# Performance work log

Hardware: AMD Instinct MI355X
Metric: run time of the kernel (lower is better)

## Reference

```python
import jax, jax.numpy as jnp
import numpy as np

B, N_OBJ, FEAT_IN = 512, 3, 2048
FEAT_SIZE = 512
EMBED = 512
HID = 512
VOCAB = 4096
MAX_LEN = 40
T = MAX_LEN - 2  # sampled steps between SOS and appended EOS
SOS_IDX, EOS_IDX = 1, 2
TAU = 1.0


def setup_inputs() -> dict:
    key = jax.random.key(0)
    ks = jax.random.split(key, 16)
    s = lambda k, shape, fan: jax.random.normal(k, shape, jnp.float32) / np.sqrt(fan)
    feats = jax.random.normal(ks[0], (B, N_OBJ, FEAT_IN), jnp.float32)
    targets = jax.random.randint(ks[1], (B,), 0, N_OBJ)
    feat_W = s(ks[2], (FEAT_SIZE, FEAT_IN), FEAT_IN)
    feat_b = jnp.zeros((FEAT_SIZE,), jnp.float32)
    emb_W = s(ks[3], (VOCAB, EMBED), EMBED)
    init_W = s(ks[4], (HID, N_OBJ * (FEAT_SIZE + 1)), N_OBJ * (FEAT_SIZE + 1))
    init_b = jnp.zeros((HID,), jnp.float32)
    gru_Wih = s(ks[5], (3 * HID, EMBED), EMBED)
    gru_Whh = s(ks[6], (3 * HID, HID), HID)
    gru_bih = jnp.zeros((3 * HID,), jnp.float32)
    gru_bhh = jnp.zeros((3 * HID,), jnp.float32)
    out_W = s(ks[7], (VOCAB, HID), HID)
    out_b = jnp.zeros((VOCAB,), jnp.float32)
    # pre-sampled gumbel noise for the T decode steps
    u = jax.random.uniform(ks[8], (T, B, VOCAB), jnp.float32, 1e-10, 1.0)
    gumbel = -jnp.log(-jnp.log(u))
    return dict(feats=feats, targets=targets, feat_W=feat_W, feat_b=feat_b,
                emb_W=emb_W, init_W=init_W, init_b=init_b,
                gru_Wih=gru_Wih, gru_Whh=gru_Whh, gru_bih=gru_bih,
                gru_bhh=gru_bhh, out_W=out_W, out_b=out_b, gumbel=gumbel)


def _gru_cell(x, h, Wih, Whh, bih, bhh):
    gi = x @ Wih.T + bih              # [B, 3H]
    gh = h @ Whh.T + bhh
    i_r, i_z, i_n = jnp.split(gi, 3, axis=-1)
    h_r, h_z, h_n = jnp.split(gh, 3, axis=-1)
    r = jax.nn.sigmoid(i_r + h_r)
    z = jax.nn.sigmoid(i_z + h_z)
    n = jnp.tanh(i_n + r * h_n)
    return (1.0 - z) * n + z * h


def _decode(feats, targets, feat_W, feat_b, emb_W, init_W, init_b,
            gru_Wih, gru_Whh, gru_bih, gru_bhh, out_W, out_b, gumbel):
    bsz = feats.shape[0]
    # embed_features: linear feat model per object + target one-hot
    fe = jnp.einsum('boi,hi->boh', feats, feat_W) + feat_b      # [B,3,F]
    t_oh = jax.nn.one_hot(targets, N_OBJ, dtype=feats.dtype)    # [B,3]
    ft = jnp.concatenate([fe, t_oh[:, :, None]], axis=2).reshape(bsz, -1)
    h0 = ft @ init_W.T + init_b                                  # [B,H]

    sos_oh = jax.nn.one_hot(jnp.full((bsz,), SOS_IDX), VOCAB, dtype=feats.dtype)
    x0 = sos_oh @ emb_W                                          # [B,E]
    done0 = jnp.zeros((bsz,), bool)
    len0 = jnp.ones((bsz,), jnp.int32)                           # counts SOS

    def step(carry, g):
        h, x, done, length = carry
        h = _gru_cell(x, h, gru_Wih, gru_Whh, gru_bih, gru_bhh)
        logits = h @ out_W.T + out_b                             # [B,V]
        soft = jax.nn.softmax((logits + g) / TAU, axis=-1)
        pred = jnp.argmax(soft, axis=-1)
        hard = jax.nn.one_hot(pred, VOCAB, dtype=soft.dtype)
        oh = hard + soft - jax.lax.stop_gradient(soft)           # straight-through
        length = length + (~done).astype(jnp.int32)
        done = done | (pred == EOS_IDX)
        x = oh @ emb_W
        return (h, x, done, length), oh

    (_, _, done, length), ohs = jax.lax.scan(step, (h0, x0, done0, len0), gumbel)
    length = length + (~done).astype(jnp.int32)                  # appended EOS

    eos_oh = jax.nn.one_hot(jnp.full((bsz,), EOS_IDX), VOCAB, dtype=feats.dtype)
    lang = jnp.concatenate(
        [sos_oh[:, None], jnp.transpose(ohs, (1, 0, 2)), eos_oh[:, None]], axis=1)
    mask = (jnp.arange(MAX_LEN)[None, :] < length[:, None])      # zero past length
    lang = lang * mask[:, :, None].astype(lang.dtype)
    return lang, length


def reference(feats, targets, feat_W, feat_b, emb_W, init_W, init_b,
              gru_Wih, gru_Whh, gru_bih, gru_bhh, out_W, out_b, gumbel):
    lang, length = _decode(feats, targets, feat_W, feat_b, emb_W, init_W, init_b,
                           gru_Wih, gru_Whh, gru_bih, gru_bhh, out_W, out_b, gumbel)
    eos_loss = jnp.float32(0.0)
    return lang, length, eos_loss
```

## Files before the change

kernel.cpp:

```cpp
#include <hip/hip_runtime.h>
#include <cstdint>
#include <cstddef>

#define BATCH   512
#define HIDDEN  512
#define EMB     512
#define VOCAB   4096
#define NOBJ    3
#define FEATIN  2048
#define FEATSZ  512
#define MAXLEN  40
#define TSTEPS  38
#define SOS     1
#define EOS     2
#define GIH     1536

#define BK 16
#define BM 64

static __device__ __forceinline__ unsigned long long pack_key(float v, int col) {
    uint32_t u = __float_as_uint(v);
    u = (u & 0x80000000u) ? ~u : (u | 0x80000000u);
    return ((unsigned long long)u << 32) | (uint32_t)(VOCAB - 1 - col);
}

__global__ __launch_bounds__(256) void k_zero(float* __restrict__ out, int n,
                                              unsigned long long* __restrict__ keys) {
    size_t i = (size_t)blockIdx.x * 256 + threadIdx.x;
    size_t i4 = i * 4;
    if (i4 + 3 < (size_t)n) {
        *(float4*)&out[i4] = make_float4(0.f, 0.f, 0.f, 0.f);
    } else if (i4 < (size_t)n) {
        for (size_t j = i4; j < (size_t)n; ++j) out[j] = 0.f;
    }
    if (i < (size_t)TSTEPS * BATCH) keys[i] = 0ULL;
}

__global__ __launch_bounds__(256) void k_fe(const float* __restrict__ feats,
                                            const float* __restrict__ featW,
                                            const float* __restrict__ featb,
                                            float* __restrict__ fe) {
    __shared__ float As[BK][BM];
    __shared__ float Bs[BK][BM];
    const int tid = threadIdx.x;
    const int m0 = blockIdx.y * BM, n0 = blockIdx.x * BM;
    const int tx = tid & 15, ty = tid >> 4;
    const int lrow = tid >> 2, lk = (tid & 3) << 2;
    float acc[4][4] = {};
    for (int k0 = 0; k0 < FEATIN; k0 += BK) {
        float4 a = *(const float4*)&feats[(size_t)(m0 + lrow) * FEATIN + k0 + lk];
        float4 b = *(const float4*)&featW[(size_t)(n0 + lrow) * FEATIN + k0 + lk];
        __syncthreads();
        As[lk+0][lrow] = a.x; As[lk+1][lrow] = a.y; As[lk+2][lrow] = a.z; As[lk+3][lrow] = a.w;
        Bs[lk+0][lrow] = b.x; Bs[lk+1][lrow] = b.y; Bs[lk+2][lrow] = b.z; Bs[lk+3][lrow] = b.w;
        __syncthreads();
#pragma unroll
        for (int kk = 0; kk < BK; ++kk) {
            float4 av = *(const float4*)&As[kk][ty * 4];
            float4 bv = *(const float4*)&Bs[kk][tx * 4];
            float ar[4] = {av.x, av.y, av.z, av.w};
            float br[4] = {bv.x, bv.y, bv.z, bv.w};
#pragma unroll
            for (int i = 0; i < 4; ++i)
#pragma unroll
                for (int j = 0; j < 4; ++j) acc[i][j] += ar[i] * br[j];
        }
    }
#pragma unroll
    for (int i = 0; i < 4; ++i) {
        int r = m0 + ty * 4 + i;
#pragma unroll
        for (int j = 0; j < 4; ++j) {
            int c = n0 + tx * 4 + j;
            fe[(size_t)r * FEATSZ + c] = acc[i][j] + featb[c];
        }
    }
}

__global__ __launch_bounds__(256) void k_h0(const float* __restrict__ fe,
                                            const float* __restrict__ initW,
                                            const float* __restrict__ initb,
                                            const int* __restrict__ targets,
                                            float* __restrict__ h) {
    __shared__ float As[BK][BM];
    __shared__ float Bs[BK][BM];
    const int tid = threadIdx.x;
    const int m0 = blockIdx.y * BM, n0 = blockIdx.x * BM;
    const int tx = tid & 15, ty = tid >> 4;
    const int lrow = tid >> 2, lk = (tid & 3) << 2;
    float acc[4][4] = {};
    const int K = NOBJ * FEATSZ;
    for (int k0 = 0; k0 < K; k0 += BK) {
        float4 a = *(const float4*)&fe[(size_t)(m0 + lrow) * K + k0 + lk];
        float breg[4];
#pragma unroll
        for (int i = 0; i < 4; ++i) {
            int ka = k0 + lk + i;
            breg[i] = initW[(size_t)(n0 + lrow) * 1539 + ka + (ka >> 9)];
        }
        __syncthreads();
        As[lk+0][lrow] = a.x; As[lk+1][lrow] = a.y; As[lk+2][lrow] = a.z; As[lk+3][lrow] = a.w;
#pragma unroll
        for (int i = 0; i < 4; ++i) Bs[lk + i][lrow] = breg[i];
        __syncthreads();
#pragma unroll
        for (int kk = 0; kk < BK; ++kk) {
            float4 av = *(const float4*)&As[kk][ty * 4];
            float4 bv = *(const float4*)&Bs[kk][tx * 4];
            float ar[4] = {av.x, av.y, av.z, av.w};
            float br[4] = {bv.x, bv.y, bv.z, bv.w};
#pragma unroll
            for (int i = 0; i < 4; ++i)
#pragma unroll
                for (int j = 0; j < 4; ++j) acc[i][j] += ar[i] * br[j];
        }
    }
#pragma unroll
    for (int i = 0; i < 4; ++i) {
        int r = m0 + ty * 4 + i;
        int tg = targets[r];
#pragma unroll
        for (int j = 0; j < 4; ++j) {
            int c = n0 + tx * 4 + j;
            h[(size_t)r * HIDDEN + c] =
                acc[i][j] + initb[c] + initW[(size_t)c * 1539 + tg * 513 + 512];
        }
    }
}

__global__ __launch_bounds__(256) void k_P(const float* __restrict__ embW,
                                           const float* __restrict__ Wih,
                                           float* __restrict__ P) {
    __shared__ __align__(16) float As[2][BK][BM + 4];
    __shared__ __align__(16) float Bs[2][BK][128 + 4];
    const int tid = threadIdx.x;
    const int arow = tid >> 2, ak = (tid & 3) << 2;
    const int tx = tid & 15, ty = tid >> 4;
    const int m0 = blockIdx.y * BM, n0 = blockIdx.x * 128;
    const float* Ap = embW + (size_t)(m0 + arow) * EMB;
    const float* Bp0 = Wih + (size_t)(n0 + arow) * EMB;
    const float* Bp1 = Wih + (size_t)(n0 + 64 + arow) * EMB;
    float4 aR = *(const float4*)&Ap[ak];
    float4 bR0 = *(const float4*)&Bp0[ak];
    float4 bR1 = *(const float4*)&Bp1[ak];
    float acc[4][8] = {};
    int buf = 0;
    for (int k0 = 0; k0 < EMB; k0 += BK) {
        As[buf][ak+0][arow] = aR.x; As[buf][ak+1][arow] = aR.y;
        As[buf][ak+2][arow] = aR.z; As[buf][ak+3][arow] = aR.w;
        Bs[buf][ak+0][arow] = bR0.x; Bs[buf][ak+1][arow] = bR0.y;
        Bs[buf][ak+2][arow] = bR0.z; Bs[buf][ak+3][arow] = bR0.w;
        Bs[buf][ak+0][arow+64] = bR1.x; Bs[buf][ak+1][arow+64] = bR1.y;
        Bs[buf][ak+2][arow+64] = bR1.z; Bs[buf][ak+3][arow+64] = bR1.w;
        __syncthreads();
        if (k0 + BK < EMB) {
            aR  = *(const float4*)&Ap[k0 + BK + ak];
            bR0 = *(const float4*)&Bp0[k0 + BK + ak];
            bR1 = *(const float4*)&Bp1[k0 + BK + ak];
        }
#pragma unroll
        for (int kk = 0; kk < BK; ++kk) {
            float4 av  = *(const float4*)&As[buf][kk][ty * 4];
            float4 bv0 = *(const float4*)&Bs[buf][kk][tx * 4];
            float4 bv1 = *(const float4*)&Bs[buf][kk][64 + tx * 4];
            float ar[4] = {av.x, av.y, av.z, av.w};
            float br[8] = {bv0.x, bv0.y, bv0.z, bv0.w, bv1.x, bv1.y, bv1.z, bv1.w};
#pragma unroll
            for (int i = 0; i < 4; ++i)
#pragma unroll
                for (int j = 0; j < 8; ++j) acc[i][j] += ar[i] * br[j];
        }
        buf ^= 1;
    }
#pragma unroll
    for (int i = 0; i < 4; ++i) {
        int r = m0 + ty * 4 + i;
        *(float4*)&P[(size_t)r * GIH + n0 + tx * 4] =
            make_float4(acc[i][0], acc[i][1], acc[i][2], acc[i][3]);
        *(float4*)&P[(size_t)r * GIH + n0 + 64 + tx * 4] =
            make_float4(acc[i][4], acc[i][5], acc[i][6], acc[i][7]);
    }
}

__global__ __launch_bounds__(256) void k_gatesH(const float* __restrict__ h,
                                                const float* __restrict__ Whh,
                                                float* __restrict__ Gh) {
    __shared__ __align__(16) float As[2][BK][BM + 4];
    __shared__ __align__(16) float Bs[2][BK][BM + 4];
    const int tid = threadIdx.x;
    const int arow = tid >> 2, ak = (tid & 3) << 2;
    const int tx = tid & 15, ty = tid >> 4;
    const int m0 = blockIdx.y * BM, n0 = blockIdx.x * BM;
    const float* Ap = h + (size_t)(m0 + arow) * HIDDEN;
    const float* Bp = Whh + (size_t)(n0 + arow) * HIDDEN;
    float4 aR = *(const float4*)&Ap[ak];
    float4 bR = *(const float4*)&Bp[ak];
    float acc[4][4] = {};
    int buf = 0;
    for (int k0 = 0; k0 < HIDDEN; k0 += BK) {
        As[buf][ak+0][arow] = aR.x; As[buf][ak+1][arow] = aR.y;
        As[buf][ak+2][arow] = aR.z; As[buf][ak+3][arow] = aR.w;
        Bs[buf][ak+0][arow] = bR.x; Bs[buf][ak+1][arow] = bR.y;
        Bs[buf][ak+2][arow] = bR.z; Bs[buf][ak+3][arow] = bR.w;
        __syncthreads();
        if (k0 + BK < HIDDEN) {
            aR = *(const float4*)&Ap[k0 + BK + ak];
            bR = *(const float4*)&Bp[k0 + BK + ak];
        }
#pragma unroll
        for (int kk = 0; kk < BK; ++kk) {
            float4 av = *(const float4*)&As[buf][kk][ty * 4];
            float4 bv = *(const float4*)&Bs[buf][kk][tx * 4];
            float ar[4] = {av.x, av.y, av.z, av.w};
            float br[4] = {bv.x, bv.y, bv.z, bv.w};
#pragma unroll
            for (int i = 0; i < 4; ++i)
#pragma unroll
                for (int j = 0; j < 4; ++j) acc[i][j] += ar[i] * br[j];
        }
        buf ^= 1;
    }
#pragma unroll
    for (int i = 0; i < 4; ++i) {
        int r = m0 + ty * 4 + i;
        *(float4*)&Gh[(size_t)r * GIH + n0 + tx * 4] =
            make_float4(acc[i][0], acc[i][1], acc[i][2], acc[i][3]);
    }
}

__global__ __launch_bounds__(256) void k_gru(const float* __restrict__ Gh,
                                             const float* __restrict__ P,
                                             const float* __restrict__ bih,
                                             const float* __restrict__ bhh,
                                             const unsigned long long* __restrict__ keys_prev,
                                             float* __restrict__ h) {
    int idx = blockIdx.x * 256 + threadIdx.x;
    int b = idx >> 7;
    int j4 = (idx & 127) << 2;
    int tok = SOS;
    if (keys_prev) tok = (VOCAB - 1) - (int)(uint32_t)(keys_prev[b] & 0xffffffffULL);
    const float* Pr = P + (size_t)tok * GIH;
    const float* Gr = Gh + (size_t)b * GIH;
    float4 ir = *(const float4*)&Pr[j4];
    float4 iz = *(const float4*)&Pr[j4 + HIDDEN];
    float4 in_ = *(const float4*)&Pr[j4 + 2 * HIDDEN];
    float4 hr = *(const float4*)&Gr[j4];
    float4 hz = *(const float4*)&Gr[j4 + HIDDEN];
    float4 hn = *(const float4*)&Gr[j4 + 2 * HIDDEN];
    float4 bir = *(const float4*)&bih[j4];
    float4 biz = *(const float4*)&bih[j4 + HIDDEN];
    float4 bin = *(const float4*)&bih[j4 + 2 * HIDDEN];
    float4 bhr = *(const float4*)&bhh[j4];
    float4 bhz = *(const float4*)&bhh[j4 + HIDDEN];
    float4 bhn = *(const float4*)&bhh[j4 + 2 * HIDDEN];
    float4 ho = *(const float4*)&h[(size_t)b * HIDDEN + j4];
    float irr[4] = {ir.x + bir.x, ir.y + bir.y, ir.z + bir.z, ir.w + bir.w};
    float izz[4] = {iz.x + biz.x, iz.y + biz.y, iz.z + biz.z, iz.w + biz.w};
    float inn[4] = {in_.x + bin.x, in_.y + bin.y, in_.z + bin.z, in_.w + bin.w};
    float hrr[4] = {hr.x + bhr.x, hr.y + bhr.y, hr.z + bhr.z, hr.w + bhr.w};
    float hzz[4] = {hz.x + bhz.x, hz.y + bhz.y, hz.z + bhz.z, hz.w + bhz.w};
    float hnn[4] = {hn.x + bhn.x, hn.y + bhn.y, hn.z + bhn.z, hn.w + bhn.w};
    float hov[4] = {ho.x, ho.y, ho.z, ho.w};
    float res[4];
#pragma unroll
    for (int i = 0; i < 4; ++i) {
        float r = 1.0f / (1.0f + expf(-(irr[i] + hrr[i])));
        float z = 1.0f / (1.0f + expf(-(izz[i] + hzz[i])));
        float n = tanhf(inn[i] + r * hnn[i]);
        res[i] = (1.0f - z) * n + z * hov[i];
    }
    *(float4*)&h[(size_t)b * HIDDEN + j4] = make_float4(res[0], res[1], res[2], res[3]);
}

__global__ __launch_bounds__(256) void k_logits(const float* __restrict__ h,
                                                const float* __restrict__ outW,
                                                const float* __restrict__ outb,
                                                const float* __restrict__ gum_t,
                                                unsigned long long* __restrict__ keys_t) {
    __shared__ __align__(16) float As[2][BK][BM + 4];
    __shared__ __align__(16) float Bs[2][BK][128 + 4];
    __shared__ unsigned long long red[BM][16];
    const int tid = threadIdx.x;
    const int arow = tid >> 2, ak = (tid & 3) << 2;
    const int tx = tid & 15, ty = tid >> 4;
    const int m0 = blockIdx.y * BM, n0 = blockIdx.x * 128;
    const float* Ap = h + (size_t)(m0 + arow) * HIDDEN;
    const float* Bp0 = outW + (size_t)(n0 + arow) * HIDDEN;
    const float* Bp1 = outW + (size_t)(n0 + 64 + arow) * HIDDEN;
    float4 aR = *(const float4*)&Ap[ak];
    float4 bR0 = *(const float4*)&Bp0[ak];
    float4 bR1 = *(const float4*)&Bp1[ak];
    float acc[4][8] = {};
    int buf = 0;
    for (int k0 = 0; k0 < HIDDEN; k0 += BK) {
        As[buf][ak+0][arow] = aR.x; As[buf][ak+1][arow] = aR.y;
        As[buf][ak+2][arow] = aR.z; As[buf][ak+3][arow] = aR.w;
        Bs[buf][ak+0][arow] = bR0.x; Bs[buf][ak+1][arow] = bR0.y;
        Bs[buf][ak+2][arow] = bR0.z; Bs[buf][ak+3][arow] = bR0.w;
        Bs[buf][ak+0][arow+64] = bR1.x; Bs[buf][ak+1][arow+64] = bR1.y;
        Bs[buf][ak+2][arow+64] = bR1.z; Bs[buf][ak+3][arow+64] = bR1.w;
        __syncthreads();
        if (k0 + BK < HIDDEN) {
            aR  = *(const float4*)&Ap[k0 + BK + ak];
            bR0 = *(const float4*)&Bp0[k0 + BK + ak];
            bR1 = *(const float4*)&Bp1[k0 + BK + ak];
        }
#pragma unroll
        for (int kk = 0; kk < BK; ++kk) {
            float4 av  = *(const float4*)&As[buf][kk][ty * 4];
            float4 bv0 = *(const float4*)&Bs[buf][kk][tx * 4];
            float4 bv1 = *(const float4*)&Bs[buf][kk][64 + tx * 4];
            float ar[4] = {av.x, av.y, av.z, av.w};
            float br[8] = {bv0.x, bv0.y, bv0.z, bv0.w, bv1.x, bv1.y, bv1.z, bv1.w};
#pragma unroll
            for (int i = 0; i < 4; ++i)
#pragma unroll
                for (int j = 0; j < 8; ++j) acc[i][j] += ar[i] * br[j];
        }
        buf ^= 1;
    }
    float4 ob0 = *(const float4*)&outb[n0 + tx * 4];
    float4 ob1 = *(const float4*)&outb[n0 + 64 + tx * 4];
    float obr[8] = {ob0.x, ob0.y, ob0.z, ob0.w, ob1.x, ob1.y, ob1.z, ob1.w};
#pragma unroll
    for (int i = 0; i < 4; ++i) {
        int r = m0 + ty * 4 + i;
        float4 g0 = *(const float4*)&gum_t[(size_t)r * VOCAB + n0 + tx * 4];
        float4 g1 = *(const float4*)&gum_t[(size_t)r * VOCAB + n0 + 64 + tx * 4];
        float gr[8] = {g0.x, g0.y, g0.z, g0.w, g1.x, g1.y, g1.z, g1.w};
        unsigned long long best = 0ULL;
#pragma unroll
        for (int j = 0; j < 8; ++j) {
            int c = n0 + ((j < 4) ? (tx * 4 + j) : (64 + tx * 4 + j - 4));
            float v = acc[i][j] + obr[j] + gr[j];
            unsigned long long key = pack_key(v, c);
            if (key > best) best = key;
        }
        red[ty * 4 + i][tx] = best;
    }
    __syncthreads();
    if (tid < BM) {
        unsigned long long best = red[tid][0];
#pragma unroll
        for (int q = 1; q < 16; ++q)
            if (red[tid][q] > best) best = red[tid][q];
        atomicMax(&keys_t[m0 + tid], best);
    }
}

__global__ __launch_bounds__(256) void k_final(const unsigned long long* __restrict__ keys,
                                               float* __restrict__ out) {
    int b = blockIdx.x * 256 + threadIdx.x;
    if (b >= BATCH) return;
    int toks[TSTEPS];
    int len = 1;
    bool done = false;
#pragma unroll
    for (int t = 0; t < TSTEPS; ++t) {
        int tok = (VOCAB - 1) - (int)(uint32_t)(keys[(size_t)t * BATCH + b] & 0xffffffffULL);
        toks[t] = tok;
        if (!done) len++;
        if (tok == EOS) done = true;
    }
    if (!done) len++;
    float* lang = out + (size_t)b * MAXLEN * VOCAB;
    lang[SOS] = 1.0f;
#pragma unroll
    for (int t = 0; t < TSTEPS; ++t) {
        int pos = t + 1;
        if (pos < len) lang[(size_t)pos * VOCAB + toks[t]] = 1.0f;
    }
    if (len == MAXLEN) lang[(size_t)(MAXLEN - 1) * VOCAB + EOS] = 1.0f;
    out[(size_t)BATCH * MAXLEN * VOCAB + b] = (float)len;
    if (b == 0) out[(size_t)BATCH * MAXLEN * VOCAB + BATCH] = 0.0f;
}

extern "C" void kernel_launch(void* const* d_in, const int* in_sizes, int n_in,
                              void* d_out, int out_size, void* d_ws, size_t ws_size,
                              hipStream_t stream) {
    const float* feats = (const float*)d_in[0];
    const int*   targets = (const int*)d_in[1];
    const float* featW = (const float*)d_in[2];
    const float* featb = (const float*)d_in[3];
    const float* embW  = (const float*)d_in[4];
    const float* initW = (const float*)d_in[5];
    const float* initb = (const float*)d_in[6];
    const float* Wih   = (const float*)d_in[7];
    const float* bih   = (const float*)d_in[9];
    const float* Whh   = (const float*)d_in[8];
    const float* bhh   = (const float*)d_in[10];
    const float* outW  = (const float*)d_in[11];
    const float* outb  = (const float*)d_in[12];
    const float* gumbel = (const float*)d_in[13];
    float* out = (float*)d_out;

    char* ws = (char*)d_ws;
    float* h  = (float*)(ws);
    float* Gh = (float*)(ws + (1 << 20));
    float* fe = (float*)(ws + 4 * (1 << 20));
    unsigned long long* keys = (unsigned long long*)(ws + 7 * (1 << 20));
    float* P  = (float*)(ws + 8 * (1 << 20));

    int zb = (out_size / 4 + 256) / 256;
    k_zero<<<dim3(zb), 256, 0, stream>>>(out, out_size, keys);

    k_fe<<<dim3(FEATSZ / BM, (BATCH * NOBJ) / BM), 256, 0, stream>>>(feats, featW, featb, fe);
    k_h0<<<dim3(HIDDEN / BM, BATCH / BM), 256, 0, stream>>>(fe, initW, initb, targets, h);
    k_P<<<dim3(GIH / 128, VOCAB / BM), 256, 0, stream>>>(embW, Wih, P);

    for (int t = 0; t < TSTEPS; ++t) {
        const unsigned long long* kprev = (t == 0) ? nullptr : (keys + (size_t)(t - 1) * BATCH);
        k_gatesH<<<dim3(GIH / BM, BATCH / BM), 256, 0, stream>>>(h, Whh, Gh);
        k_gru<<<dim3(BATCH * HIDDEN / 4 / 256), 256, 0, stream>>>(Gh, P, bih, bhh, kprev, h);
        k_logits<<<dim3(VOCAB / 128, BATCH / BM), 256, 0, stream>>>(
            h, outW, outb, gumbel + (size_t)t * BATCH * VOCAB, keys + (size_t)t * BATCH);
    }
    k_final<<<dim3(2), 256, 0, stream>>>(keys, out);
}
```

Before: 3.204 ms.

## Fuse logits and next-step hidden gate GEMMs into one launch with split-K

Merges the output-logits GEMM with argmax and the next step's h@Whh gate GEMM into one combined kernel. The first 512 blocks compute logits and the remaining 384 compute the hidden gates with K split in two, writing partial sums that the GRU kernel adds. This cuts one launch per step and fills the GPU better, since the gates GEMM alone had few blocks. It also folds bih into the precomputed token table, uses smaller logits tiles, and gives k_zero more work per thread. The cost is extra partial-sum traffic and a changed workspace layout in which fe aliases Gp.

```diff
diff --git a/kernel.cpp b/kernel.cpp
--- a/kernel.cpp
+++ b/kernel.cpp
@@ -14,9 +14,14 @@
 #define SOS     1
 #define EOS     2
 #define GIH     1536
+#define KCH     256
 
 #define BK 16
 #define BM 64
+
+#define NLOGITS_BLK 512
+#define NGATES_BLK  384
+#define NCOMB_BLK   (NLOGITS_BLK + NGATES_BLK)
 
 static __device__ __forceinline__ unsigned long long pack_key(float v, int col) {
     uint32_t u = __float_as_uint(v);
@@ -26,14 +31,19 @@
 
 __global__ __launch_bounds__(256) void k_zero(float* __restrict__ out, int n,
                                               unsigned long long* __restrict__ keys) {
-    size_t i = (size_t)blockIdx.x * 256 + threadIdx.x;
-    size_t i4 = i * 4;
-    if (i4 + 3 < (size_t)n) {
-        *(float4*)&out[i4] = make_float4(0.f, 0.f, 0.f, 0.f);
-    } else if (i4 < (size_t)n) {
-        for (size_t j = i4; j < (size_t)n; ++j) out[j] = 0.f;
-    }
-    if (i < (size_t)TSTEPS * BATCH) keys[i] = 0ULL;
+    int tid = threadIdx.x;
+    size_t base = (size_t)blockIdx.x * 4096;
+#pragma unroll
+    for (int s = 0; s < 4; ++s) {
+        size_t i4 = base + (size_t)s * 1024 + (size_t)tid * 4;
+        if (i4 + 3 < (size_t)n) {
+            *(float4*)&out[i4] = make_float4(0.f, 0.f, 0.f, 0.f);
+        } else {
+            for (size_t j = i4; j < (size_t)n; ++j) out[j] = 0.f;
+        }
+    }
+    size_t gi = (size_t)blockIdx.x * 256 + tid;
+    if (gi < (size_t)TSTEPS * BATCH) keys[gi] = 0ULL;
 }
 
 __global__ __launch_bounds__(256) void k_fe(const float* __restrict__ feats,
@@ -130,6 +140,7 @@
 
 __global__ __launch_bounds__(256) void k_P(const float* __restrict__ embW,
                                            const float* __restrict__ Wih,
+                                           const float* __restrict__ bih,
                                            float* __restrict__ P) {
     __shared__ __align__(16) float As[2][BK][BM + 4];
     __shared__ __align__(16) float Bs[2][BK][128 + 4];
@@ -172,65 +183,138 @@
         }
         buf ^= 1;
     }
+    float4 bi0 = *(const float4*)&bih[n0 + tx * 4];
+    float4 bi1 = *(const float4*)&bih[n0 + 64 + tx * 4];
 #pragma unroll
     for (int i = 0; i < 4; ++i) {
         int r = m0 + ty * 4 + i;
         *(float4*)&P[(size_t)r * GIH + n0 + tx * 4] =
-            make_float4(acc[i][0], acc[i][1], acc[i][2], acc[i][3]);
+            make_float4(acc[i][0] + bi0.x, acc[i][1] + bi0.y, acc[i][2] + bi0.z, acc[i][3] + bi0.w);
         *(float4*)&P[(size_t)r * GIH + n0 + 64 + tx * 4] =
-            make_float4(acc[i][4], acc[i][5], acc[i][6], acc[i][7]);
-    }
-}
-
-__global__ __launch_bounds__(256) void k_gatesH(const float* __restrict__ h,
-                                                const float* __restrict__ Whh,
-                                                float* __restrict__ Gh) {
+            make_float4(acc[i][4] + bi1.x, acc[i][5] + bi1.y, acc[i][6] + bi1.z, acc[i][7] + bi1.w);
+    }
+}
+
+__global__ __launch_bounds__(256) void k_comb(const float* __restrict__ h,
+                                              const float* __restrict__ Whh,
+                                              float* __restrict__ Gp,
+                                              const float* __restrict__ outW,
+                                              const float* __restrict__ outb,
+                                              const float* __restrict__ gum_t,
+                                              unsigned long long* __restrict__ keys_t,
+                                              int do_logits, int do_gates) {
     __shared__ __align__(16) float As[2][BK][BM + 4];
     __shared__ __align__(16) float Bs[2][BK][BM + 4];
+    __shared__ unsigned long long red[BM][16];
     const int tid = threadIdx.x;
     const int arow = tid >> 2, ak = (tid & 3) << 2;
     const int tx = tid & 15, ty = tid >> 4;
-    const int m0 = blockIdx.y * BM, n0 = blockIdx.x * BM;
-    const float* Ap = h + (size_t)(m0 + arow) * HIDDEN;
-    const float* Bp = Whh + (size_t)(n0 + arow) * HIDDEN;
-    float4 aR = *(const float4*)&Ap[ak];
-    float4 bR = *(const float4*)&Bp[ak];
-    float acc[4][4] = {};
-    int buf = 0;
-    for (int k0 = 0; k0 < HIDDEN; k0 += BK) {
-        As[buf][ak+0][arow] = aR.x; As[buf][ak+1][arow] = aR.y;
-        As[buf][ak+2][arow] = aR.z; As[buf][ak+3][arow] = aR.w;
-        Bs[buf][ak+0][arow] = bR.x; Bs[buf][ak+1][arow] = bR.y;
-        Bs[buf][ak+2][arow] = bR.z; Bs[buf][ak+3][arow] = bR.w;
-        __syncthreads();
-        if (k0 + BK < HIDDEN) {
-            aR = *(const float4*)&Ap[k0 + BK + ak];
-            bR = *(const float4*)&Bp[k0 + BK + ak];
-        }
-#pragma unroll
-        for (int kk = 0; kk < BK; ++kk) {
-            float4 av = *(const float4*)&As[buf][kk][ty * 4];
-            float4 bv = *(const float4*)&Bs[buf][kk][tx * 4];
-            float ar[4] = {av.x, av.y, av.z, av.w};
-            float br[4] = {bv.x, bv.y, bv.z, bv.w};
-#pragma unroll
-            for (int i = 0; i < 4; ++i)
-#pragma unroll
-                for (int j = 0; j < 4; ++j) acc[i][j] += ar[i] * br[j];
-        }
-        buf ^= 1;
-    }
-#pragma unroll
-    for (int i = 0; i < 4; ++i) {
-        int r = m0 + ty * 4 + i;
-        *(float4*)&Gh[(size_t)r * GIH + n0 + tx * 4] =
-            make_float4(acc[i][0], acc[i][1], acc[i][2], acc[i][3]);
-    }
-}
-
-__global__ __launch_bounds__(256) void k_gru(const float* __restrict__ Gh,
+    const int bx = blockIdx.x;
+
+    if (bx < NLOGITS_BLK) {
+        if (!do_logits) return;
+        const int n0 = (bx & 63) * 64, m0 = (bx >> 6) * 64;
+        const float* Ap = h + (size_t)(m0 + arow) * HIDDEN;
+        const float* Bp = outW + (size_t)(n0 + arow) * HIDDEN;
+        float4 aR = *(const float4*)&Ap[ak];
+        float4 bR = *(const float4*)&Bp[ak];
+        float acc[4][4] = {};
+        int buf = 0;
+        for (int k0 = 0; k0 < HIDDEN; k0 += BK) {
+            As[buf][ak+0][arow] = aR.x; As[buf][ak+1][arow] = aR.y;
+            As[buf][ak+2][arow] = aR.z; As[buf][ak+3][arow] = aR.w;
+            Bs[buf][ak+0][arow] = bR.x; Bs[buf][ak+1][arow] = bR.y;
+            Bs[buf][ak+2][arow] = bR.z; Bs[buf][ak+3][arow] = bR.w;
+            __syncthreads();
+            if (k0 + BK < HIDDEN) {
+                aR = *(const float4*)&Ap[k0 + BK + ak];
+                bR = *(const float4*)&Bp[k0 + BK + ak];
+            }
+#pragma unroll
+            for (int kk = 0; kk < BK; ++kk) {
+                float4 av = *(const float4*)&As[buf][kk][ty * 4];
+                float4 bv = *(const float4*)&Bs[buf][kk][tx * 4];
+                float ar[4] = {av.x, av.y, av.z, av.w};
+                float br[4] = {bv.x, bv.y, bv.z, bv.w};
+#pragma unroll
+                for (int i = 0; i < 4; ++i)
+#pragma unroll
+                    for (int j = 0; j < 4; ++j) acc[i][j] += ar[i] * br[j];
+            }
+            buf ^= 1;
+        }
+        float4 ob = *(const float4*)&outb[n0 + tx * 4];
+        float obr[4] = {ob.x, ob.y, ob.z, ob.w};
+#pragma unroll
+        for (int i = 0; i < 4; ++i) {
+            int r = m0 + ty * 4 + i;
+            float4 g = *(const float4*)&gum_t[(size_t)r * VOCAB + n0 + tx * 4];
+            float gr[4] = {g.x, g.y, g.z, g.w};
+            unsigned long long best = 0ULL;
+#pragma unroll
+            for (int j = 0; j < 4; ++j) {
+                int c = n0 + tx * 4 + j;
+                unsigned long long key = pack_key(acc[i][j] + obr[j] + gr[j], c);
+                if (key > best) best = key;
+            }
+            red[ty * 4 + i][tx] = best;
+        }
+        __syncthreads();
+        if (tid < BM) {
+            unsigned long long best = red[tid][0];
+#pragma unroll
+            for (int q = 1; q < 16; ++q)
+                if (red[tid][q] > best) best = red[tid][q];
+            atomicMax(&keys_t[m0 + tid], best);
+        }
+    } else {
+        if (!do_gates) return;
+        const int gx = bx - NLOGITS_BLK;
+        const int jn = gx % 24;
+        const int rest = gx / 24;
+        const int jm = rest & 7, kc = rest >> 3;
+        const int m0 = jm * 64, n0 = jn * 64;
+        const float* Ap = h + (size_t)(m0 + arow) * HIDDEN + kc * KCH;
+        const float* Bp = Whh + (size_t)(n0 + arow) * HIDDEN + kc * KCH;
+        float4 aR = *(const float4*)&Ap[ak];
+        float4 bR = *(const float4*)&Bp[ak];
+        float acc[4][4] = {};
+        int buf = 0;
+        for (int k0 = 0; k0 < KCH; k0 += BK) {
+            As[buf][ak+0][arow] = aR.x; As[buf][ak+1][arow] = aR.y;
+            As[buf][ak+2][arow] = aR.z; As[buf][ak+3][arow] = aR.w;
+            Bs[buf][ak+0][arow] = bR.x; Bs[buf][ak+1][arow] = bR.y;
+            Bs[buf][ak+2][arow] = bR.z; Bs[buf][ak+3][arow] = bR.w;
+            __syncthreads();
+            if (k0 + BK < KCH) {
+                aR = *(const float4*)&Ap[k0 + BK + ak];
+                bR = *(const float4*)&Bp[k0 + BK + ak];
+            }
+#pragma unroll
+            for (int kk = 0; kk < BK; ++kk) {
+                float4 av = *(const float4*)&As[buf][kk][ty * 4];
+                float4 bv = *(const float4*)&Bs[buf][kk][tx * 4];
+                float ar[4] = {av.x, av.y, av.z, av.w};
+                float br[4] = {bv.x, bv.y, bv.z, bv.w};
+#pragma unroll
+                for (int i = 0; i < 4; ++i)
+#pragma unroll
+                    for (int j = 0; j < 4; ++j) acc[i][j] += ar[i] * br[j];
+            }
+            buf ^= 1;
+        }
+        float* Go = Gp + (size_t)(kc * BATCH) * GIH;
+#pragma unroll
+        for (int i = 0; i < 4; ++i) {
+            int r = m0 + ty * 4 + i;
+            *(float4*)&Go[(size_t)r * GIH + n0 + tx * 4] =
+                make_float4(acc[i][0], acc[i][1], acc[i][2], acc[i][3]);
+        }
+    }
+}
+
+__global__ __launch_bounds__(256) void k_gru(const float* __restrict__ Gp,
                                              const float* __restrict__ P,
-                                             const float* __restrict__ bih,
                                              const float* __restrict__ bhh,
                                              const unsigned long long* __restrict__ keys_prev,
                                              float* __restrict__ h) {
@@ -240,26 +324,30 @@
     int tok = SOS;
     if (keys_prev) tok = (VOCAB - 1) - (int)(uint32_t)(keys_prev[b] & 0xffffffffULL);
     const float* Pr = P + (size_t)tok * GIH;
-    const float* Gr = Gh + (size_t)b * GIH;
+    const float* G0 = Gp + (size_t)b * GIH;
+    const float* G1 = Gp + (size_t)(BATCH + b) * GIH;
     float4 ir = *(const float4*)&Pr[j4];
     float4 iz = *(const float4*)&Pr[j4 + HIDDEN];
     float4 in_ = *(const float4*)&Pr[j4 + 2 * HIDDEN];
-    float4 hr = *(const float4*)&Gr[j4];
-    float4 hz = *(const float4*)&Gr[j4 + HIDDEN];
-    float4 hn = *(const float4*)&Gr[j4 + 2 * HIDDEN];
-    float4 bir = *(const float4*)&bih[j4];
-    float4 biz = *(const float4*)&bih[j4 + HIDDEN];
-    float4 bin = *(const float4*)&bih[j4 + 2 * HIDDEN];
+    float4 hr0 = *(const float4*)&G0[j4];
+    float4 hz0 = *(const float4*)&G0[j4 + HIDDEN];
+    float4 hn0 = *(const float4*)&G0[j4 + 2 * HIDDEN];
+    float4 hr1 = *(const float4*)&G1[j4];
+    float4 hz1 = *(const float4*)&G1[j4 + HIDDEN];
+    float4 hn1 = *(const float4*)&G1[j4 + 2 * HIDDEN];
     float4 bhr = *(const float4*)&bhh[j4];
     float4 bhz = *(const float4*)&bhh[j4 + HIDDEN];
     float4 bhn = *(const float4*)&bhh[j4 + 2 * HIDDEN];
     float4 ho = *(const float4*)&h[(size_t)b * HIDDEN + j4];
-    float irr[4] = {ir.x + bir.x, ir.y + bir.y, ir.z + bir.z, ir.w + bir.w};
-    float izz[4] = {iz.x + biz.x, iz.y + biz.y, iz.z + biz.z, iz.w + biz.w};
-    float inn[4] = {in_.x + bin.x, in_.y + bin.y, in_.z + bin.z, in_.w + bin.w};
-    float hrr[4] = {hr.x + bhr.x, hr.y + bhr.y, hr.z + bhr.z, hr.w + bhr.w};
-    float hzz[4] = {hz.x + bhz.x, hz.y + bhz.y, hz.z + bhz.z, hz.w + bhz.w};
-    float hnn[4] = {hn.x + bhn.x, hn.y + bhn.y, hn.z + bhn.z, hn.w + bhn.w};
+    float irr[4] = {ir.x, ir.y, ir.z, ir.w};
+    float izz[4] = {iz.x, iz.y, iz.z, iz.w};
+    float inn[4] = {in_.x, in_.y, in_.z, in_.w};
+    float hrr[4] = {hr0.x + hr1.x + bhr.x, hr0.y + hr1.y + bhr.y,
+                    hr0.z + hr1.z + bhr.z, hr0.w + hr1.w + bhr.w};
+    float hzz[4] = {hz0.x + hz1.x + bhz.x, hz0.y + hz1.y + bhz.y,
+                    hz0.z + hz1.z + bhz.z, hz0.w + hz1.w + bhz.w};
+    float hnn[4] = {hn0.x + hn1.x + bhn.x, hn0.y + hn1.y + bhn.y,
+                    hn0.z + hn1.z + bhn.z, hn0.w + hn1.w + bhn.w};
     float hov[4] = {ho.x, ho.y, ho.z, ho.w};
     float res[4];
 #pragma unroll
@@ -270,82 +358,6 @@
         res[i] = (1.0f - z) * n + z * hov[i];
     }
     *(float4*)&h[(size_t)b * HIDDEN + j4] = make_float4(res[0], res[1], res[2], res[3]);
-}
-
-__global__ __launch_bounds__(256) void k_logits(const float* __restrict__ h,
-                                                const float* __restrict__ outW,
-                                                const float* __restrict__ outb,
-                                                const float* __restrict__ gum_t,
-                                                unsigned long long* __restrict__ keys_t) {
-    __shared__ __align__(16) float As[2][BK][BM + 4];
-    __shared__ __align__(16) float Bs[2][BK][128 + 4];
-    __shared__ unsigned long long red[BM][16];
-    const int tid = threadIdx.x;
-    const int arow = tid >> 2, ak = (tid & 3) << 2;
-    const int tx = tid & 15, ty = tid >> 4;
-    const int m0 = blockIdx.y * BM, n0 = blockIdx.x * 128;
-    const float* Ap = h + (size_t)(m0 + arow) * HIDDEN;
-    const float* Bp0 = outW + (size_t)(n0 + arow) * HIDDEN;
-    const float* Bp1 = outW + (size_t)(n0 + 64 + arow) * HIDDEN;
-    float4 aR = *(const float4*)&Ap[ak];
-    float4 bR0 = *(const float4*)&Bp0[ak];
-    float4 bR1 = *(const float4*)&Bp1[ak];
-    float acc[4][8] = {};
-    int buf = 0;
-    for (int k0 = 0; k0 < HIDDEN; k0 += BK) {
-        As[buf][ak+0][arow] = aR.x; As[buf][ak+1][arow] = aR.y;
-        As[buf][ak+2][arow] = aR.z; As[buf][ak+3][arow] = aR.w;
-        Bs[buf][ak+0][arow] = bR0.x; Bs[buf][ak+1][arow] = bR0.y;
-        Bs[buf][ak+2][arow] = bR0.z; Bs[buf][ak+3][arow] = bR0.w;
-        Bs[buf][ak+0][arow+64] = bR1.x; Bs[buf][ak+1][arow+64] = bR1.y;
-        Bs[buf][ak+2][arow+64] = bR1.z; Bs[buf][ak+3][arow+64] = bR1.w;
-        __syncthreads();
-        if (k0 + BK < HIDDEN) {
-            aR  = *(const float4*)&Ap[k0 + BK + ak];
-            bR0 = *(const float4*)&Bp0[k0 + BK + ak];
-            bR1 = *(const float4*)&Bp1[k0 + BK + ak];
-        }
-#pragma unroll
-        for (int kk = 0; kk < BK; ++kk) {
-            float4 av  = *(const float4*)&As[buf][kk][ty * 4];
-            float4 bv0 = *(const float4*)&Bs[buf][kk][tx * 4];
-            float4 bv1 = *(const float4*)&Bs[buf][kk][64 + tx * 4];
-            float ar[4] = {av.x, av.y, av.z, av.w};
-            float br[8] = {bv0.x, bv0.y, bv0.z, bv0.w, bv1.x, bv1.y, bv1.z, bv1.w};
-#pragma unroll
-            for (int i = 0; i < 4; ++i)
-#pragma unroll
-                for (int j = 0; j < 8; ++j) acc[i][j] += ar[i] * br[j];
-        }
-        buf ^= 1;
-    }
-    float4 ob0 = *(const float4*)&outb[n0 + tx * 4];
-    float4 ob1 = *(const float4*)&outb[n0 + 64 + tx * 4];
-    float obr[8] = {ob0.x, ob0.y, ob0.z, ob0.w, ob1.x, ob1.y, ob1.z, ob1.w};
-#pragma unroll
-    for (int i = 0; i < 4; ++i) {
-        int r = m0 + ty * 4 + i;
-        float4 g0 = *(const float4*)&gum_t[(size_t)r * VOCAB + n0 + tx * 4];
-        float4 g1 = *(const float4*)&gum_t[(size_t)r * VOCAB + n0 + 64 + tx * 4];
-        float gr[8] = {g0.x, g0.y, g0.z, g0.w, g1.x, g1.y, g1.z, g1.w};
-        unsigned long long best = 0ULL;
-#pragma unroll
-        for (int j = 0; j < 8; ++j) {
-            int c = n0 + ((j < 4) ? (tx * 4 + j) : (64 + tx * 4 + j - 4));
-            float v = acc[i][j] + obr[j] + gr[j];
-            unsigned long long key = pack_key(v, c);
-            if (key > best) best = key;
-        }
-        red[ty * 4 + i][tx] = best;
-    }
-    __syncthreads();
-    if (tid < BM) {
-        unsigned long long best = red[tid][0];
-#pragma unroll
-        for (int q = 1; q < 16; ++q)
-            if (red[tid][q] > best) best = red[tid][q];
-        atomicMax(&keys_t[m0 + tid], best);
-    }
 }
 
 __global__ __launch_bounds__(256) void k_final(const unsigned long long* __restrict__ keys,
@@ -386,8 +398,8 @@
     const float* initW = (const float*)d_in[5];
     const float* initb = (const float*)d_in[6];
     const float* Wih   = (const float*)d_in[7];
+    const float* Whh   = (const float*)d_in[8];
     const float* bih   = (const float*)d_in[9];
-    const float* Whh   = (const float*)d_in[8];
     const float* bhh   = (const float*)d_in[10];
     const float* outW  = (const float*)d_in[11];
     const float* outb  = (const float*)d_in[12];
@@ -396,24 +408,26 @@
 
     char* ws = (char*)d_ws;
     float* h  = (float*)(ws);
-    float* Gh = (float*)(ws + (1 << 20));
-    float* fe = (float*)(ws + 4 * (1 << 20));
-    unsigned long long* keys = (unsigned long long*)(ws + 7 * (1 << 20));
+    unsigned long long* keys = (unsigned long long*)(ws + (1 << 20));
+    float* Gp = (float*)(ws + 5 * (1 << 18));
+    float* fe = Gp;
     float* P  = (float*)(ws + 8 * (1 << 20));
 
-    int zb = (out_size / 4 + 256) / 256;
+    int zb = (out_size + 4095) / 4096;
     k_zero<<<dim3(zb), 256, 0, stream>>>(out, out_size, keys);
 
     k_fe<<<dim3(FEATSZ / BM, (BATCH * NOBJ) / BM), 256, 0, stream>>>(feats, featW, featb, fe);
     k_h0<<<dim3(HIDDEN / BM, BATCH / BM), 256, 0, stream>>>(fe, initW, initb, targets, h);
-    k_P<<<dim3(GIH / 128, VOCAB / BM), 256, 0, stream>>>(embW, Wih, P);
+    k_P<<<dim3(GIH / 128, VOCAB / BM), 256, 0, stream>>>(embW, Wih, bih, P);
+
+    k_comb<<<dim3(NCOMB_BLK), 256, 0, stream>>>(h, Whh, Gp, outW, outb, gumbel, keys, 0, 1);
 
     for (int t = 0; t < TSTEPS; ++t) {
         const unsigned long long* kprev = (t == 0) ? nullptr : (keys + (size_t)(t - 1) * BATCH);
-        k_gatesH<<<dim3(GIH / BM, BATCH / BM), 256, 0, stream>>>(h, Whh, Gh);
-        k_gru<<<dim3(BATCH * HIDDEN / 4 / 256), 256, 0, stream>>>(Gh, P, bih, bhh, kprev, h);
-        k_logits<<<dim3(VOCAB / 128, BATCH / BM), 256, 0, stream>>>(
-            h, outW, outb, gumbel + (size_t)t * BATCH * VOCAB, keys + (size_t)t * BATCH);
+        k_gru<<<dim3(BATCH * HIDDEN / 4 / 256), 256, 0, stream>>>(Gp, P, bhh, kprev, h);
+        k_comb<<<dim3(NCOMB_BLK), 256, 0, stream>>>(
+            h, Whh, Gp, outW, outb, gumbel + (size_t)t * BATCH * VOCAB,
+            keys + (size_t)t * BATCH, 1, (t < TSTEPS - 1) ? 1 : 0);
     }
     k_final<<<dim3(2), 256, 0, stream>>>(keys, out);
 }
```

New measurement: 2.656 ms. 1.21x faster.
